# Kernel optimization log

Hardware: AMD Instinct MI355X
Metric: run time of the kernel (lower is better)

## Reference

```python
import jax, jax.numpy as jnp
import numpy as np

B, T, C = 4, 2048, 1024
N_HEADS = 16
HEAD_DIM = C // N_HEADS


def rotary_embedding(seq_len, dim, dtype=jnp.float32):
    pos = jnp.arange(seq_len, dtype=dtype)[:, None]
    i = jnp.arange(0, dim, 2, dtype=dtype)[None, :]
    theta = pos / jnp.power(10000.0, i / dim)
    return jnp.cos(theta), jnp.sin(theta)


def apply_rotary(x, cos, sin):
    # x: [B, T, H, D]; cos/sin: [T, D//2]
    d = x.shape[-1]
    x1, x2 = x[..., : d // 2], x[..., d // 2 :]
    rotated = jnp.concatenate([-x2, x1], axis=-1)
    cos = jnp.concatenate([cos, cos], axis=-1)[None, :, None, :]
    sin = jnp.concatenate([sin, sin], axis=-1)[None, :, None, :]
    return x * cos + rotated * sin


def setup_inputs() -> dict:
    key = jax.random.key(0)
    k1, k2, k3 = jax.random.split(key, 3)
    x = jax.random.normal(k1, (B, T, C), dtype=jnp.float32)
    # lecun_normal-ish init scale
    w_qkv = jax.random.normal(k2, (C, 3 * C), dtype=jnp.float32) / np.sqrt(C)
    w_out = jax.random.normal(k3, (C, C), dtype=jnp.float32) / np.sqrt(C)
    return {"x": x, "w_qkv": w_qkv, "w_out": w_out}


def reference(x, w_qkv, w_out):
    b, t, c = x.shape
    qkv = jnp.einsum("btc,cd->btd", x, w_qkv)
    q, k, v = jnp.split(qkv, 3, axis=-1)
    q = q.reshape(b, t, N_HEADS, HEAD_DIM)
    k = k.reshape(b, t, N_HEADS, HEAD_DIM)
    v = v.reshape(b, t, N_HEADS, HEAD_DIM)
    cos, sin = rotary_embedding(t, HEAD_DIM, dtype=x.dtype)
    q = apply_rotary(q, cos, sin)
    k = apply_rotary(k, cos, sin)
    scale = jnp.sqrt(jnp.asarray(HEAD_DIM, dtype=x.dtype))
    # scores: [B, H, T, T]
    attn = jnp.einsum("bqhd,bkhd->bhqk", q, k) / scale
    mask = jnp.tril(jnp.ones((t, t), dtype=jnp.bool_))
    attn = jnp.where(mask[None, None, :, :], attn, jnp.asarray(-1e9, dtype=x.dtype))
    attn = jax.nn.softmax(attn, axis=-1)
    out = jnp.einsum("bhqk,bkhd->bqhd", attn, v).reshape(b, t, c)
    return jnp.einsum("btc,cd->btd", out, w_out)
```

## Files before the change

### kernel.cpp

```cpp
#include <hip/hip_runtime.h>
#include <stdint.h>

#define DEVI __device__ __forceinline__

typedef unsigned short ushort_t;
typedef __bf16 bf16x8 __attribute__((ext_vector_type(8)));
typedef float f32x4 __attribute__((ext_vector_type(4)));
typedef unsigned short ushort8 __attribute__((ext_vector_type(8)));
typedef short s16x4 __attribute__((ext_vector_type(4)));

#define BB 4
#define TT 2048
#define CC 1024
#define NH 16
#define HD 64
#define MM (BB*TT)

DEVI ushort_t f2bf(float f) {
    __bf16 h = (__bf16)f;
    return __builtin_bit_cast(ushort_t, h);
}

typedef const __attribute__((address_space(1))) unsigned int guint_t;
typedef __attribute__((address_space(3))) unsigned int luint_t;

DEVI void gl2lds16(const void* g, void* lds) {
    __builtin_amdgcn_global_load_lds((guint_t*)(uintptr_t)g,
                                     (luint_t*)(unsigned int)(uintptr_t)lds,
                                     16, 0, 0);
}

template <int N> DEVI void waitvm() {
    static_assert(N == 0 || N == 6 || N == 8, "unsupported vmcnt literal");
    if constexpr (N == 0)      asm volatile("s_waitcnt vmcnt(0)" ::: "memory");
    else if constexpr (N == 6) asm volatile("s_waitcnt vmcnt(6)" ::: "memory");
    else if constexpr (N == 8) asm volatile("s_waitcnt vmcnt(8)" ::: "memory");
}

__global__ void cvt_f32_bf16(const float* __restrict__ in,
                             ushort_t* __restrict__ out) {
    int i = blockIdx.x * 256 + threadIdx.x;
    const float4* p = (const float4*)in + (size_t)i * 2;
    float4 a = p[0], b = p[1];
    ushort8 r;
    r[0] = f2bf(a.x); r[1] = f2bf(a.y); r[2] = f2bf(a.z); r[3] = f2bf(a.w);
    r[4] = f2bf(b.x); r[5] = f2bf(b.y); r[6] = f2bf(b.z); r[7] = f2bf(b.w);
    *(ushort8*)(out + (size_t)i * 8) = r;
}

__global__ void transpose_f2b(const float* __restrict__ in,
                              ushort_t* __restrict__ out, int R, int Cc) {
    __shared__ ushort_t tile[32][33];
    int bx = blockIdx.x * 32;
    int by = blockIdx.y * 32;
    int tx = threadIdx.x & 31, ty = threadIdx.x >> 5;
    #pragma unroll
    for (int i = 0; i < 4; i++) {
        int r = ty * 4 + i;
        tile[r][tx] = f2bf(in[(size_t)(by + r) * Cc + bx + tx]);
    }
    __syncthreads();
    #pragma unroll
    for (int i = 0; i < 4; i++) {
        int r = ty * 4 + i;
        out[(size_t)(bx + r) * R + by + tx] = tile[tx][r];
    }
}

__global__ void rope_table(float2* __restrict__ tab) {
    int i = blockIdx.x * 256 + threadIdx.x;
    int t = i >> 5, j = i & 31;
    float inv = exp2f((float)j * -0.41524101186092029f);
    float theta = (float)t * inv;
    float s, c;
    sincosf(theta, &s, &c);
    tab[i] = make_float2(c, s);
}

__global__ void vtrans(const ushort_t* __restrict__ Vb,
                       ushort_t* __restrict__ VbT) {
    __shared__ ushort_t tile[64 * 72];
    const int bh = blockIdx.y;
    const int t0 = blockIdx.x * 64;
    const int tid = threadIdx.x;
    const int r = tid >> 2, c = (tid & 3) * 16;
    const size_t base = (size_t)bh * (TT * HD);
    const ushort_t* g = Vb + base + (size_t)(t0 + r) * HD + c;
    *(ushort8*)&tile[r * 72 + c]     = *(const ushort8*)g;
    *(ushort8*)&tile[r * 72 + c + 8] = *(const ushort8*)(g + 8);
    __syncthreads();
    ushort8 a, b;
    #pragma unroll
    for (int j = 0; j < 8; j++) a[j] = tile[(c + j) * 72 + r];
    #pragma unroll
    for (int j = 0; j < 8; j++) b[j] = tile[(c + 8 + j) * 72 + r];
    ushort_t* o = VbT + base + (size_t)r * TT + t0 + c;
    *(ushort8*)o = a;
    *(ushort8*)(o + 8) = b;
}

template <int MODE, int BM>
__global__ __launch_bounds__(512, 2) void gemm_bt(
    const ushort_t* __restrict__ A, const ushort_t* __restrict__ Bt,
    float* __restrict__ CoutF,
    ushort_t* __restrict__ Qb, ushort_t* __restrict__ Kb, ushort_t* __restrict__ Vb,
    const float2* __restrict__ rope, int M, int N, int Kd) {
    constexpr int MR = BM / 32;
    constexpr int AL = BM / 64;
    constexpr int L  = AL + 4;
    constexpr int NK = CC / 64;
    (void)M;

    __shared__ __attribute__((aligned(16))) ushort_t As[2][BM * 64];
    __shared__ __attribute__((aligned(16))) ushort_t Bs[2][256 * 64];

    const int tid = threadIdx.x;
    const int w = tid >> 6, l = tid & 63;
    const int lane15 = l & 15, quad = l >> 4;
    const int wm = (w >> 2) * (BM / 2);
    const int wn = (w & 3) * 64;

    const int nbn = gridDim.x;
    const int nwg = nbn * gridDim.y;
    const int lid = blockIdx.y * nbn + blockIdx.x;
    const int sid = (lid & 7) * (nwg >> 3) + (lid >> 3);
    const int bn = sid % nbn, bm = sid / nbn;

    const int sr8 = l >> 3;
    const int sc  = l & 7;

    auto STAGE = [&](int buf, int k0) {
        #pragma unroll
        for (int i = 0; i < AL; ++i) {
            int r = w * (BM / 8) + i * 8 + sr8;
            int gr = bm * BM + r;
            size_t e;
            if constexpr (MODE == 2)
                e = ((size_t)(gr >> 11)) * 2097152 + ((size_t)(k0 >> 6)) * 131072
                    + (size_t)(gr & (TT - 1)) * 64;
            else
                e = (size_t)gr * Kd + k0;
            const char* g = (const char*)(A + e) + ((sc ^ sr8) * 16);
            gl2lds16(g, (char*)&As[buf][0] + (w * (BM / 8) + i * 8) * 128);
        }
        #pragma unroll
        for (int i = 0; i < 4; ++i) {
            int r = w * 32 + i * 8 + sr8;
            int gr = bn * 256 + r;
            const char* g = (const char*)(Bt + (size_t)gr * Kd + k0)
                            + ((sc ^ sr8) * 16);
            gl2lds16(g, (char*)&Bs[buf][0] + (w * 32 + i * 8) * 128);
        }
    };

    f32x4 acc[MR][4];
    #pragma unroll
    for (int m = 0; m < MR; ++m)
        #pragma unroll
        for (int n = 0; n < 4; ++n)
            acc[m][n] = f32x4{0.f, 0.f, 0.f, 0.f};

    STAGE(0, 0);
    STAGE(1, 64);
    waitvm<L>();
    __builtin_amdgcn_s_barrier();
    asm volatile("" ::: "memory");

    const int swz = (lane15 & 7) << 4;

    for (int k = 0; k < NK; ++k) {
        const char* Asb = (const char*)&As[k & 1][0];
        const char* Bsb = (const char*)&Bs[k & 1][0];
        #pragma unroll
        for (int kk = 0; kk < 2; ++kk) {
            const int cb = (kk * 64 + quad * 16) ^ swz;
            bf16x8 bfr[4];
            #pragma unroll
            for (int n = 0; n < 4; ++n)
                bfr[n] = *(const bf16x8*)(Bsb + (wn + n * 16 + lane15) * 128 + cb);
            bf16x8 af[MR];
            #pragma unroll
            for (int m = 0; m < MR; ++m)
                af[m] = *(const bf16x8*)(Asb + (wm + m * 16 + lane15) * 128 + cb);
            __builtin_amdgcn_s_setprio(1);
            #pragma unroll
            for (int m = 0; m < MR; ++m)
                #pragma unroll
                for (int n = 0; n < 4; ++n)
                    acc[m][n] = __builtin_amdgcn_mfma_f32_16x16x32_bf16(
                        af[m], bfr[n], acc[m][n], 0, 0, 0);
            __builtin_amdgcn_s_setprio(0);
        }
        if (k == NK - 1) break;

        __builtin_amdgcn_sched_barrier(0);
        asm volatile("s_waitcnt lgkmcnt(0)" ::: "memory");
        __builtin_amdgcn_s_barrier();
        asm volatile("" ::: "memory");
        if (k + 2 < NK) { STAGE(k & 1, (k + 2) * 64); waitvm<L>(); }
        else            waitvm<0>();
        __builtin_amdgcn_s_barrier();
        asm volatile("" ::: "memory");
    }

    if constexpr (MODE == 1) {
        const float SCQ = 0.125f * 1.4426950408889634f;
        const int colbase = bn * 256 + wn;
        const int seg = colbase >> 10;
        const int h = (colbase & 1023) >> 6;
        #pragma unroll
        for (int m = 0; m < MR; ++m) {
            int row0 = bm * BM + wm + m * 16 + quad * 4;
            #pragma unroll
            for (int r = 0; r < 4; ++r) {
                int row = row0 + r;
                int b = row >> 11, t = row & (TT - 1);
                size_t ob = ((size_t)(b * NH + h) * TT + t) * HD;
                if (seg == 2) {
                    #pragma unroll
                    for (int n = 0; n < 4; ++n)
                        Vb[ob + n * 16 + lane15] = f2bf(acc[m][n][r]);
                } else {
                    ushort_t* dst = (seg == 0) ? Qb : Kb;
                    #pragma unroll
                    for (int n = 0; n < 2; ++n) {
                        int j = n * 16 + lane15;
                        float2 cs = rope[t * 32 + j];
                        float x1 = acc[m][n][r];
                        float x2 = acc[m][n + 2][r];
                        float y1 = x1 * cs.x - x2 * cs.y;
                        float y2 = x2 * cs.x + x1 * cs.y;
                        if (seg == 0) { y1 *= SCQ; y2 *= SCQ; }
                        dst[ob + j]      = f2bf(y1);
                        dst[ob + 32 + j] = f2bf(y2);
                    }
                }
            }
        }
    } else {
        #pragma unroll
        for (int m = 0; m < MR; ++m) {
            #pragma unroll
            for (int r = 0; r < 4; ++r) {
                size_t rb = (size_t)(bm * BM + wm + m * 16 + quad * 4 + r) * N
                            + bn * 256 + wn;
                #pragma unroll
                for (int n = 0; n < 4; ++n)
                    CoutF[rb + n * 16 + lane15] = acc[m][n][r];
            }
        }
    }
}

__global__ __launch_bounds__(512, 4) void attn_kernel(
    ushort_t* __restrict__ Qb, const ushort_t* __restrict__ Kb,
    const ushort_t* __restrict__ VbT) {
    __shared__ __attribute__((aligned(16))) ushort_t Ks[64 * 72];
    __shared__ __attribute__((aligned(16))) ushort_t Vs[64 * 72];

    const int tid = threadIdx.x;
    const int w = tid >> 6, l = tid & 63;
    const int lane15 = l & 15, quad = l >> 4;

    const int d = blockIdx.y * gridDim.x + blockIdx.x;
    const int xcd = d & 7, j = d >> 3;
    const int bh = xcd * 8 + (j & 7);
    const int qt = 15 - (j >> 3);
    const size_t base = (size_t)bh * (TT * HD);

    const int sr = tid >> 3;
    const int sd = (tid & 7) * 8;
    const ushort_t* kgb = Kb  + base + (size_t)sr * HD + sd;
    const ushort_t* vgb = VbT + base + (size_t)sr * TT + sd;

    const int q0 = qt * 128;
    const int rbase = q0 + w * 16;
    const int ktmax = 2 * qt + 1;

    bf16x8 qf0, qf1;
    {
        const ushort_t* qp = Qb + base + (size_t)(rbase + lane15) * HD + quad * 8;
        qf0 = *(const bf16x8*)qp;
        qf1 = *(const bf16x8*)(qp + 32);
    }

    f32x4 o[4];
    #pragma unroll
    for (int nt = 0; nt < 4; nt++) o[nt] = f32x4{0.f, 0.f, 0.f, 0.f};
    float mrow = -INFINITY, lrow = 0.f;

    ushort8 kr = *(const ushort8*)kgb;
    ushort8 vr = *(const ushort8*)vgb;

    for (int kt = 0; kt <= ktmax; kt++) {
        __syncthreads();
        *(ushort8*)&Ks[sr * 72 + sd] = kr;
        *(ushort8*)&Vs[sr * 72 + sd] = vr;
        __syncthreads();
        if (kt < ktmax) {
            kr = *(const ushort8*)(kgb + (size_t)(kt + 1) * 64 * HD);
            vr = *(const ushort8*)(vgb + (size_t)(kt + 1) * 64);
        }

        if (kt * 64 > rbase + 15) continue;

        f32x4 s[4];
        #pragma unroll
        for (int c = 0; c < 4; c++) {
            bf16x8 k0 = *(const bf16x8*)&Ks[(c * 16 + lane15) * 72 + quad * 8];
            bf16x8 k1 = *(const bf16x8*)&Ks[(c * 16 + lane15) * 72 + 32 + quad * 8];
            f32x4 z = f32x4{0.f, 0.f, 0.f, 0.f};
            z = __builtin_amdgcn_mfma_f32_16x16x32_bf16(k0, qf0, z, 0, 0, 0);
            s[c] = __builtin_amdgcn_mfma_f32_16x16x32_bf16(k1, qf1, z, 0, 0, 0);
        }

        const int qrow = rbase + lane15;
        if (kt * 64 + 63 > rbase) {
            #pragma unroll
            for (int c = 0; c < 4; c++)
                #pragma unroll
                for (int r = 0; r < 4; r++)
                    if (kt * 64 + c * 16 + quad * 4 + r > qrow) s[c][r] = -1e9f;
        }

        float mt = s[0][0];
        #pragma unroll
        for (int c = 0; c < 4; c++)
            #pragma unroll
            for (int r = 0; r < 4; r++) mt = fmaxf(mt, s[c][r]);
        mt = fmaxf(mt, __shfl_xor(mt, 16, 64));
        mt = fmaxf(mt, __shfl_xor(mt, 32, 64));

        float alpha = 1.0f;
        if (!__all(mt - mrow <= 8.0f)) {
            float mn = fmaxf(mrow, mt);
            alpha = __builtin_amdgcn_exp2f(mrow - mn);
            mrow = mn;
            #pragma unroll
            for (int r = 0; r < 4; r++) {
                float aO = __shfl(alpha, quad * 4 + r, 64);
                #pragma unroll
                for (int nt = 0; nt < 4; nt++) o[nt][r] *= aO;
            }
        }

        #pragma unroll
        for (int c = 0; c < 4; c++)
            #pragma unroll
            for (int r = 0; r < 4; r++)
                s[c][r] = __builtin_amdgcn_exp2f(s[c][r] - mrow);

        float rs = 0.f;
        #pragma unroll
        for (int c = 0; c < 4; c++)
            rs += (s[c][0] + s[c][1]) + (s[c][2] + s[c][3]);
        rs += __shfl_xor(rs, 16, 64);
        rs += __shfl_xor(rs, 32, 64);
        lrow = lrow * alpha + rs;

        #pragma unroll
        for (int c = 0; c < 4; c++) {
            s16x4 pf;
            #pragma unroll
            for (int r = 0; r < 4; r++) pf[r] = (short)f2bf(s[c][r]);
            #pragma unroll
            for (int nt = 0; nt < 4; nt++) {
                s16x4 vf = *(const s16x4*)&Vs[(nt * 16 + lane15) * 72 +
                                              c * 16 + quad * 4];
                o[nt] = __builtin_amdgcn_mfma_f32_16x16x16bf16_1k(
                    pf, vf, o[nt], 0, 0, 0);
            }
        }
    }

    float linv = 1.0f / lrow;
    #pragma unroll
    for (int r = 0; r < 4; r++) {
        float lO = __shfl(linv, quad * 4 + r, 64);
        size_t rb = base + (size_t)(rbase + quad * 4 + r) * HD;
        #pragma unroll
        for (int nt = 0; nt < 4; nt++)
            Qb[rb + nt * 16 + lane15] = f2bf(o[nt][r] * lO);
    }
}

extern "C" void kernel_launch(void* const* d_in, const int* in_sizes, int n_in,
                              void* d_out, int out_size, void* d_ws, size_t ws_size,
                              hipStream_t stream) {
    const float* x    = (const float*)d_in[0];
    const float* wqkv = (const float*)d_in[1];
    const float* wout = (const float*)d_in[2];
    float* out = (float*)d_out;

    char* ws = (char*)d_ws;
    ushort_t* WqkvT = (ushort_t*)(ws);
    ushort_t* WoutT = (ushort_t*)(ws + 6291456);
    float2*   rope  = (float2*)  (ws + 8388608);
    ushort_t* Xb    = (ushort_t*)(ws + 8912896);
    ushort_t* Qb    = (ushort_t*)(ws + 8912896 + 16777216);
    ushort_t* Kb    = (ushort_t*)(ws + 8912896 + 2 * 16777216);
    ushort_t* Vb    = (ushort_t*)(ws + 8912896 + 3 * 16777216);
    ushort_t* VbT   = Xb;

    cvt_f32_bf16<<<dim3(MM * CC / (256 * 8)), 256, 0, stream>>>(x, Xb);
    transpose_f2b<<<dim3(3 * CC / 32, CC / 32), 256, 0, stream>>>(wqkv, WqkvT, CC, 3 * CC);
    transpose_f2b<<<dim3(CC / 32, CC / 32), 256, 0, stream>>>(wout, WoutT, CC, CC);
    rope_table<<<dim3(256), 256, 0, stream>>>(rope);

    gemm_bt<1, 128><<<dim3(3 * CC / 256, MM / 128), 512, 0, stream>>>(
        Xb, WqkvT, nullptr, Qb, Kb, Vb, rope, MM, 3 * CC, CC);

    vtrans<<<dim3(TT / 64, BB * NH), 256, 0, stream>>>(Vb, VbT);

    attn_kernel<<<dim3(16, BB * NH), 512, 0, stream>>>(Qb, Kb, VbT);

    gemm_bt<2, 128><<<dim3(CC / 256, MM / 128), 512, 0, stream>>>(
        Qb, WoutT, out, nullptr, nullptr, nullptr, nullptr, MM, CC, CC);
}
```

Baseline: 270.8 us.

## Double-buffer attention K/V tiles, compute row sums via MFMA, reorder q-tile scheduling

The attention kernel now keeps two LDS buffers for K and V, so the next tile is stored while the current one is consumed, and needs only one barrier per iteration instead of two. The softmax row sum is accumulated by an MFMA against a ones vector, using the same bf16-rounded probabilities as the PV product, which drops the cross-lane shuffle reductions. The row max shuffle is now done only when a rescale is needed. The query-tile order per block comes from a fixed permutation, mixing heavy and light causal tiles for load balance. LDS use doubles, which may limit occupancy.

```diff
diff --git a/kernel.cpp b/kernel.cpp
--- a/kernel.cpp
+++ b/kernel.cpp
@@ -255,8 +255,8 @@
 __global__ __launch_bounds__(512, 4) void attn_kernel(
     ushort_t* __restrict__ Qb, const ushort_t* __restrict__ Kb,
     const ushort_t* __restrict__ VbT) {
-    __shared__ __attribute__((aligned(16))) ushort_t Ks[64 * 72];
-    __shared__ __attribute__((aligned(16))) ushort_t Vs[64 * 72];
+    __shared__ __attribute__((aligned(16))) ushort_t Ks[2][64 * 72];
+    __shared__ __attribute__((aligned(16))) ushort_t Vs[2][64 * 72];
 
     const int tid = threadIdx.x;
     const int w = tid >> 6, l = tid & 63;
@@ -265,7 +265,7 @@
     const int d = blockIdx.y * gridDim.x + blockIdx.x;
     const int xcd = d & 7, j = d >> 3;
     const int bh = xcd * 8 + (j & 7);
-    const int qt = 15 - (j >> 3);
+    const int qt = (int)((0x765489AB3210CDEFull >> (4 * (j >> 3))) & 15);
     const size_t base = (size_t)bh * (TT * HD);
 
     const int sr = tid >> 3;
@@ -287,96 +287,98 @@
     f32x4 o[4];
     #pragma unroll
     for (int nt = 0; nt < 4; nt++) o[nt] = f32x4{0.f, 0.f, 0.f, 0.f};
-    float mrow = -INFINITY, lrow = 0.f;
+    f32x4 lacc = f32x4{0.f, 0.f, 0.f, 0.f};
+    float mrow = -INFINITY;
+
+    const s16x4 ONES = {(short)0x3F80, (short)0x3F80,
+                        (short)0x3F80, (short)0x3F80};
 
     ushort8 kr = *(const ushort8*)kgb;
     ushort8 vr = *(const ushort8*)vgb;
+    *(ushort8*)&Ks[0][sr * 72 + sd] = kr;
+    *(ushort8*)&Vs[0][sr * 72 + sd] = vr;
+    kr = *(const ushort8*)(kgb + (size_t)64 * HD);
+    vr = *(const ushort8*)(vgb + 64);
+    __syncthreads();
 
     for (int kt = 0; kt <= ktmax; kt++) {
-        __syncthreads();
-        *(ushort8*)&Ks[sr * 72 + sd] = kr;
-        *(ushort8*)&Vs[sr * 72 + sd] = vr;
-        __syncthreads();
+        const int buf = kt & 1;
         if (kt < ktmax) {
-            kr = *(const ushort8*)(kgb + (size_t)(kt + 1) * 64 * HD);
-            vr = *(const ushort8*)(vgb + (size_t)(kt + 1) * 64);
-        }
-
-        if (kt * 64 > rbase + 15) continue;
-
-        f32x4 s[4];
-        #pragma unroll
-        for (int c = 0; c < 4; c++) {
-            bf16x8 k0 = *(const bf16x8*)&Ks[(c * 16 + lane15) * 72 + quad * 8];
-            bf16x8 k1 = *(const bf16x8*)&Ks[(c * 16 + lane15) * 72 + 32 + quad * 8];
-            f32x4 z = f32x4{0.f, 0.f, 0.f, 0.f};
-            z = __builtin_amdgcn_mfma_f32_16x16x32_bf16(k0, qf0, z, 0, 0, 0);
-            s[c] = __builtin_amdgcn_mfma_f32_16x16x32_bf16(k1, qf1, z, 0, 0, 0);
-        }
-
-        const int qrow = rbase + lane15;
-        if (kt * 64 + 63 > rbase) {
-            #pragma unroll
-            for (int c = 0; c < 4; c++)
+            *(ushort8*)&Ks[buf ^ 1][sr * 72 + sd] = kr;
+            *(ushort8*)&Vs[buf ^ 1][sr * 72 + sd] = vr;
+        }
+        if (kt + 2 <= ktmax) {
+            kr = *(const ushort8*)(kgb + (size_t)(kt + 2) * 64 * HD);
+            vr = *(const ushort8*)(vgb + (size_t)(kt + 2) * 64);
+        }
+
+        if (kt * 64 <= rbase + 15) {
+            f32x4 s[4];
+            #pragma unroll
+            for (int c = 0; c < 4; c++) {
+                bf16x8 k0 = *(const bf16x8*)&Ks[buf][(c * 16 + lane15) * 72 + quad * 8];
+                bf16x8 k1 = *(const bf16x8*)&Ks[buf][(c * 16 + lane15) * 72 + 32 + quad * 8];
+                f32x4 z = f32x4{0.f, 0.f, 0.f, 0.f};
+                z = __builtin_amdgcn_mfma_f32_16x16x32_bf16(k0, qf0, z, 0, 0, 0);
+                s[c] = __builtin_amdgcn_mfma_f32_16x16x32_bf16(k1, qf1, z, 0, 0, 0);
+            }
+
+            const int qrow = rbase + lane15;
+            if (kt * 64 + 63 > rbase) {
+                #pragma unroll
+                for (int c = 0; c < 4; c++)
+                    #pragma unroll
+                    for (int r = 0; r < 4; r++)
+                        if (kt * 64 + c * 16 + quad * 4 + r > qrow) s[c][r] = -1e9f;
+            }
+
+            float a0 = fmaxf(fmaxf(s[0][0], s[0][1]), s[0][2]);
+            float a1 = fmaxf(fmaxf(s[0][3], s[1][0]), s[1][1]);
+            float a2 = fmaxf(fmaxf(s[1][2], s[1][3]), s[2][0]);
+            float a3 = fmaxf(fmaxf(s[2][1], s[2][2]), s[2][3]);
+            float a4 = fmaxf(fmaxf(s[3][0], s[3][1]), s[3][2]);
+            float mt = fmaxf(fmaxf(a0, a1), a2);
+            mt = fmaxf(fmaxf(mt, a3), fmaxf(a4, s[3][3]));
+
+            if (!__all(mt - mrow <= 8.0f)) {
+                float mf = fmaxf(mt, __shfl_xor(mt, 16, 64));
+                mf = fmaxf(mf, __shfl_xor(mf, 32, 64));
+                float mn = fmaxf(mrow, mf);
+                float alpha = __builtin_amdgcn_exp2f(mrow - mn);
+                mrow = mn;
+                #pragma unroll
+                for (int r = 0; r < 4; r++) {
+                    float aO = __shfl(alpha, quad * 4 + r, 64);
+                    #pragma unroll
+                    for (int nt = 0; nt < 4; nt++) o[nt][r] *= aO;
+                    lacc[r] *= aO;
+                }
+            }
+
+            #pragma unroll
+            for (int c = 0; c < 4; c++) {
+                s16x4 pf;
                 #pragma unroll
                 for (int r = 0; r < 4; r++)
-                    if (kt * 64 + c * 16 + quad * 4 + r > qrow) s[c][r] = -1e9f;
-        }
-
-        float mt = s[0][0];
-        #pragma unroll
-        for (int c = 0; c < 4; c++)
-            #pragma unroll
-            for (int r = 0; r < 4; r++) mt = fmaxf(mt, s[c][r]);
-        mt = fmaxf(mt, __shfl_xor(mt, 16, 64));
-        mt = fmaxf(mt, __shfl_xor(mt, 32, 64));
-
-        float alpha = 1.0f;
-        if (!__all(mt - mrow <= 8.0f)) {
-            float mn = fmaxf(mrow, mt);
-            alpha = __builtin_amdgcn_exp2f(mrow - mn);
-            mrow = mn;
-            #pragma unroll
-            for (int r = 0; r < 4; r++) {
-                float aO = __shfl(alpha, quad * 4 + r, 64);
-                #pragma unroll
-                for (int nt = 0; nt < 4; nt++) o[nt][r] *= aO;
-            }
-        }
-
-        #pragma unroll
-        for (int c = 0; c < 4; c++)
-            #pragma unroll
-            for (int r = 0; r < 4; r++)
-                s[c][r] = __builtin_amdgcn_exp2f(s[c][r] - mrow);
-
-        float rs = 0.f;
-        #pragma unroll
-        for (int c = 0; c < 4; c++)
-            rs += (s[c][0] + s[c][1]) + (s[c][2] + s[c][3]);
-        rs += __shfl_xor(rs, 16, 64);
-        rs += __shfl_xor(rs, 32, 64);
-        lrow = lrow * alpha + rs;
-
-        #pragma unroll
-        for (int c = 0; c < 4; c++) {
-            s16x4 pf;
-            #pragma unroll
-            for (int r = 0; r < 4; r++) pf[r] = (short)f2bf(s[c][r]);
-            #pragma unroll
-            for (int nt = 0; nt < 4; nt++) {
-                s16x4 vf = *(const s16x4*)&Vs[(nt * 16 + lane15) * 72 +
-                                              c * 16 + quad * 4];
-                o[nt] = __builtin_amdgcn_mfma_f32_16x16x16bf16_1k(
-                    pf, vf, o[nt], 0, 0, 0);
-            }
-        }
-    }
-
-    float linv = 1.0f / lrow;
+                    pf[r] = (short)f2bf(__builtin_amdgcn_exp2f(s[c][r] - mrow));
+                lacc = __builtin_amdgcn_mfma_f32_16x16x16bf16_1k(
+                    pf, ONES, lacc, 0, 0, 0);
+                #pragma unroll
+                for (int nt = 0; nt < 4; nt++) {
+                    s16x4 vf = *(const s16x4*)&Vs[buf][(nt * 16 + lane15) * 72 +
+                                                      c * 16 + quad * 4];
+                    o[nt] = __builtin_amdgcn_mfma_f32_16x16x16bf16_1k(
+                        pf, vf, o[nt], 0, 0, 0);
+                }
+            }
+        }
+
+        if (kt < ktmax) __syncthreads();
+    }
+
     #pragma unroll
     for (int r = 0; r < 4; r++) {
-        float lO = __shfl(linv, quad * 4 + r, 64);
+        float lO = 1.0f / lacc[r];
         size_t rb = base + (size_t)(rbase + quad * 4 + r) * HD;
         #pragma unroll
         for (int nt = 0; nt < 4; nt++)
```

After: 264.4 us. 2.4% less time.
